# Kernel optimization log

Measured on AMD Instinct MI355X. Metric: run time of the kernel, lower is better.

## Reference

```python
import jax, jax.numpy as jnp
from jax import lax
import numpy as np

DN = ('NDHWC', 'DHWIO', 'NDHWC')

def conv3d(x, w, b, stride=1):
    return lax.conv_general_dilated(x, w, (stride,) * 3, 'SAME', dimension_numbers=DN) + b

def convT3d(x, w, b, stride=2):
    return lax.conv_transpose(x, w, (stride,) * 3, 'SAME', dimension_numbers=DN) + b

def prelu(x, a):
    return jnp.where(x > 0, x, a * x)

def bn(x, g, be, m, v):
    # keras BatchNormalization, inference mode, epsilon=1e-3
    return (x - m) * g * lax.rsqrt(v + 1e-3) + be

def res_unit(x, c1w, c1b, c2w, c2b, g, be, m, v, a):
    # VQVAEResidualUnit: relu(x + PReLU(BN(conv2(swish(conv1(x))))))
    h = jax.nn.swish(conv3d(x, c1w, c1b))
    h = prelu(bn(conv3d(h, c2w, c2b), g, be, m, v), a)
    return jax.nn.relu(x + h)

def _forward(x, ec0_w, ec0_b, er0_c1w, er0_c1b, er0_c2w, er0_c2b, er0_g, er0_be, er0_m, er0_v, er0_a, ec1_w, ec1_b, er1_c1w, er1_c1b, er1_c2w, er1_c2b, er1_g, er1_be, er1_m, er1_v, er1_a, eo_w, eo_b, eo_a, codebook, dc0_w, dc0_b, dc0_a, dr0_c1w, dr0_c1b, dr0_c2w, dr0_c2b, dr0_g, dr0_be, dr0_m, dr0_v, dr0_a, du0_w, du0_b, dr1_c1w, dr1_c1b, dr1_c2w, dr1_c2b, dr1_g, dr1_be, dr1_m, dr1_v, dr1_a, du1_w, du1_b):
    # ----- Encoder -----
    h = jax.nn.relu(conv3d(x, ec0_w, ec0_b, stride=2))   # [B,64,64,64,64]
    h = res_unit(h, er0_c1w, er0_c1b, er0_c2w, er0_c2b, er0_g, er0_be, er0_m, er0_v, er0_a)
    h = jax.nn.relu(conv3d(h, ec1_w, ec1_b, stride=2))   # [B,32,32,32,128]
    h = res_unit(h, er1_c1w, er1_c1b, er1_c2w, er1_c2b, er1_g, er1_be, er1_m, er1_v, er1_a)
    z = prelu(conv3d(h, eo_w, eo_b), eo_a)               # [B,32,32,32,64] latent
    # ----- NSVQ (inference: hard codebook lookup) -----
    D = z.shape[-1]
    flat = z.reshape(-1, D)                              # [N, 64], N = B*32^3
    dist = (flat * flat).sum(1, keepdims=True) + (codebook * codebook).sum(1) - 2.0 * (flat @ codebook.T)  # [N, K]
    idx = jnp.argmin(dist, axis=1)
    zq = codebook[idx].reshape(z.shape)
    K = codebook.shape[0]
    p = jnp.zeros((K,), jnp.float32).at[idx].add(1.0) / flat.shape[0]
    perplexity = jnp.exp(-jnp.sum(p * jnp.log(p + 1e-12)))
    # ----- Decoder -----
    h = prelu(conv3d(zq, dc0_w, dc0_b), dc0_a)           # [B,32,32,32,128]
    h = res_unit(h, dr0_c1w, dr0_c1b, dr0_c2w, dr0_c2b, dr0_g, dr0_be, dr0_m, dr0_v, dr0_a)
    h = jax.nn.relu(convT3d(h, du0_w, du0_b))            # [B,64,64,64,64]
    h = res_unit(h, dr1_c1w, dr1_c1b, dr1_c2w, dr1_c2b, dr1_g, dr1_be, dr1_m, dr1_v, dr1_a)
    recon = convT3d(h, du1_w, du1_b)                     # [B,128,128,128,1]
    return recon, perplexity

def setup_inputs() -> dict:
    key = jax.random.key(0)
    ks = iter(jax.random.split(key, 40))
    nrm = lambda *s: jax.random.normal(next(ks), s, jnp.float32) * 0.05
    def ru(pfx, c):
        return {pfx + '_c1w': nrm(3, 3, 3, c, c), pfx + '_c1b': jnp.zeros((c,), jnp.float32),
                pfx + '_c2w': nrm(3, 3, 3, c, c), pfx + '_c2b': jnp.zeros((c,), jnp.float32),
                pfx + '_g': jnp.ones((c,), jnp.float32), pfx + '_be': jnp.zeros((c,), jnp.float32),
                pfx + '_m': jnp.zeros((c,), jnp.float32), pfx + '_v': jnp.ones((c,), jnp.float32),
                pfx + '_a': jnp.full((c,), 0.25, jnp.float32)}
    C0, C1, D, K = 64, 128, 64, 512
    inp = {'x': jax.random.normal(next(ks), (2, 128, 128, 128, 1), jnp.float32)}
    inp.update(ec0_w=nrm(4, 4, 4, 1, C0), ec0_b=jnp.zeros((C0,), jnp.float32))
    inp.update(ru('er0', C0))
    inp.update(ec1_w=nrm(4, 4, 4, C0, C1), ec1_b=jnp.zeros((C1,), jnp.float32))
    inp.update(ru('er1', C1))
    inp.update(eo_w=nrm(3, 3, 3, C1, D), eo_b=jnp.zeros((D,), jnp.float32), eo_a=jnp.full((D,), 0.25, jnp.float32))
    inp.update(codebook=jax.random.uniform(next(ks), (K, D), jnp.float32, -1.0, 1.0) * np.sqrt(6.0 / D).astype(np.float32))
    inp.update(dc0_w=nrm(3, 3, 3, D, C1), dc0_b=jnp.zeros((C1,), jnp.float32), dc0_a=jnp.full((C1,), 0.25, jnp.float32))
    inp.update(ru('dr0', C1))
    inp.update(du0_w=nrm(4, 4, 4, C1, C0), du0_b=jnp.zeros((C0,), jnp.float32))
    inp.update(ru('dr1', C0))
    inp.update(du1_w=nrm(4, 4, 4, C0, 1), du1_b=jnp.zeros((1,), jnp.float32))
    return inp

def reference(x, ec0_w, ec0_b, er0_c1w, er0_c1b, er0_c2w, er0_c2b, er0_g, er0_be, er0_m, er0_v, er0_a, ec1_w, ec1_b, er1_c1w, er1_c1b, er1_c2w, er1_c2b, er1_g, er1_be, er1_m, er1_v, er1_a, eo_w, eo_b, eo_a, codebook, dc0_w, dc0_b, dc0_a, dr0_c1w, dr0_c1b, dr0_c2w, dr0_c2b, dr0_g, dr0_be, dr0_m, dr0_v, dr0_a, du0_w, du0_b, dr1_c1w, dr1_c1b, dr1_c2w, dr1_c2b, dr1_g, dr1_be, dr1_m, dr1_v, dr1_a, du1_w, du1_b):
    return _forward(x, ec0_w, ec0_b, er0_c1w, er0_c1b, er0_c2w, er0_c2b, er0_g, er0_be, er0_m, er0_v, er0_a, ec1_w, ec1_b, er1_c1w, er1_c1b, er1_c2w, er1_c2b, er1_g, er1_be, er1_m, er1_v, er1_a, eo_w, eo_b, eo_a, codebook, dc0_w, dc0_b, dc0_a, dr0_c1w, dr0_c1b, dr0_c2w, dr0_c2b, dr0_g, dr0_be, dr0_m, dr0_v, dr0_a, du0_w, du0_b, dr1_c1w, dr1_c1b, dr1_c2w, dr1_c2b, dr1_g, dr1_be, dr1_m, dr1_v, dr1_a, du1_w, du1_b)
```

## Files before the change

kernel.cpp:

```cpp
#include <hip/hip_runtime.h>
#include <cstdint>


typedef unsigned short bf16_t;
typedef __attribute__((ext_vector_type(8)))  short s8b;
typedef __attribute__((ext_vector_type(16))) float f32x16;

__device__ __forceinline__ float b2f(bf16_t u) { return __uint_as_float((unsigned)u << 16); }
__device__ __forceinline__ bf16_t f2b(float f) {
    unsigned x = __float_as_uint(f);
    return (bf16_t)((x + 0x7FFFu + ((x >> 16) & 1u)) >> 16);
}

__device__ __forceinline__ void split3s(float v, unsigned short& h,
                                        unsigned short& m, unsigned short& l)
{
    const unsigned uv = __float_as_uint(v);
    const float fh = __uint_as_float(uv & 0xFFFF0000u);
    const float r1 = v - fh;
    const unsigned u1 = __float_as_uint(r1);
    const float fm = __uint_as_float(u1 & 0xFFFF0000u);
    const float r2 = r1 - fm;
    h = (unsigned short)(uv >> 16);
    m = (unsigned short)(u1 >> 16);
// ... 8 lines not shown

__global__ __launch_bounds__(256)
void wprep3(const float* __restrict__ w, bf16_t* __restrict__ h,
            bf16_t* __restrict__ m, bf16_t* __restrict__ l,
            int ci, int co, int n)
{
    const int i = blockIdx.x * 256 + threadIdx.x;
    if (i >= n) return;
    const int co_ = i % co;
    const int ci_ = (i / co) % ci;
    const int tap = i / (co * ci);
    const int dst = wdst(tap, ci_, co_, ci, co);
    unsigned short hh, mm, ll2;
    split3s(w[i], hh, mm, ll2);
    h[dst] = hh; m[dst] = mm; l[dst] = ll2;
}

__global__ __launch_bounds__(256)
void wprep_split(const float* __restrict__ w, bf16_t* __restrict__ hi,
                 bf16_t* __restrict__ lo, int ci, int co, int n)
{
    const int i = blockIdx.x * 256 + threadIdx.x;
    if (i >= n) return;
    const int co_ = i % co;
    const int ci_ = (i / co) % ci;
    const int tap = i / (co * ci);
    const float v = w[i];
    const int dst = wdst(tap, ci_, co_, ci, co);
    const bf16_t h = f2b(v);
    hi[dst] = h;
    lo[dst] = f2b(v - b2f(h));
}

template<int CIN, int COUT, int SD, int NWC, int EPI>
__global__ __launch_bounds__((SD / 32) * NWC * 64)
void conv3e(const float* __restrict__ xf,
            const bf16_t* __restrict__ wh, const bf16_t* __restrict__ wm,
            const bf16_t* __restrict__ wl,
            const float* __restrict__ bias,
            const float* __restrict__ g, const float* __restrict__ be,
            const float* __restrict__ mn, const float* __restrict__ vr,
            const float* __restrict__ al,
            const float* skf, float* __restrict__ of)
{
    constexpr int NT = (SD / 32) * NWC * 64;
    constexpr int LP = (SD * CIN) / (4 * NT);
    constexpr int KS = CIN / 16;
    constexpr int RB = (SD + 2) * CIN;
    __shared__ bf16_t lh[2][RB], lm[2][RB], ll[2][RB];

    const int tid  = threadIdx.x;
    const int lane = tid & 63;
    const int wid  = tid >> 6;
    const int wn   = wid % NWC, wm2 = wid / NWC;
    const int half = lane >> 5, ln = lane & 31;
    const int w    = wm2 * 32 + ln;
    const int nwg  = gridDim.x;
    const int bid  = (blockIdx.x & 7) * (nwg >> 3) + (blockIdx.x >> 3);
    const int h    = bid % SD;
    const int d    = (bid / SD) % SD;
    const int b    = bid / (SD * SD);
    const int cout = wn * 32 + ln;

    int pz[9], py[9], pt[9], np = 0;
    for (int kd = 0; kd < 3; ++kd) {
        const int iz = d + kd - 1;
        if ((unsigned)iz >= (unsigned)SD) continue;
        for (int kh = 0; kh < 3; ++kh) {
            const int iy = h + kh - 1;
            if ((unsigned)iy >= (unsigned)SD) continue;
            pz[np] = iz; py[np] = iy; pt[np] = (kd * 3 + kh) * 3; ++np;
        }
    }

    f32x16 accA, accB;
#pragma unroll
    for (int i = 0; i < 16; ++i) { accA[i] = 0.f; accB[i] = 0.f; }

    for (int i = tid; i < CIN; i += NT) {
        const int bf2 = i / (CIN / 2);
        const int rem = i % (CIN / 2);
        const int pv = (rem < CIN / 4) ? 0 : (SD + 1);
        const int ch = (rem % (CIN / 4)) * 4;
        const int bo = ((pv * CIN + ch) * 2) ^ ((pv & 7) << 4);
        const ushort4 z4 = make_ushort4(0, 0, 0, 0);
        *reinterpret_cast<ushort4*>((char*)&lh[bf2][0] + bo) = z4;
        *reinterpret_cast<ushort4*>((char*)&lm[bf2][0] + bo) = z4;
        *reinterpret_cast<ushort4*>((char*)&ll[bf2][0] + bo) = z4;
    }

    float4 rg[LP];
    auto loadrow = [&](int iz, int iy) {
        const float* src = xf + ((size_t)((b * SD + iz) * SD + iy)) * SD * CIN;
#pragma unroll
        for (int j = 0; j < LP; ++j)
            rg[j] = *reinterpret_cast<const float4*>(src + (size_t)(tid + j * NT) * 4);
    };
    auto writerow = [&](int bf2) {
#pragma unroll
        for (int j = 0; j < LP; ++j) {
            const int idx = (tid + j * NT) * 4;
            const int pv = idx / CIN + 1, ch = idx % CIN;
            ushort4 h4, m4, l4;
            split3s(rg[j].x, h4.x, m4.x, l4.x);
            split3s(rg[j].y, h4.y, m4.y, l4.y);
            split3s(rg[j].z, h4.z, m4.z, l4.z);
            split3s(rg[j].w, h4.w, m4.w, l4.w);
            const int bo = ((pv * CIN + ch) * 2) ^ ((pv & 7) << 4);
            *reinterpret_cast<ushort4*>((char*)&lh[bf2][0] + bo) = h4;
            *reinterpret_cast<ushort4*>((char*)&lm[bf2][0] + bo) = m4;
            *reinterpret_cast<ushort4*>((char*)&ll[bf2][0] + bo) = l4;
        }
    };

    loadrow(pz[0], py[0]);
    writerow(0);
    if (np > 1) loadrow(pz[1], py[1]);
    __syncthreads();
#pragma unroll 1
    for (int i = 0; i < np; ++i) {
        const int cur = i & 1;
        if (i + 1 < np) writerow((i + 1) & 1);
        if (i + 2 < np) loadrow(pz[i + 2], py[i + 2]);
#pragma unroll
        for (int kw = 0; kw < 3; ++kw) {
            const int tap = pt[i] + kw;
            const int pv = w + kw;
#pragma unroll
            for (int ks = 0; ks < KS; ++ks) {
                const int bo = ((pv * CIN + half * 8 + ks * 16) * 2) ^ ((pv & 7) << 4);
                const s8b ah  = *reinterpret_cast<const s8b*>((const char*)&lh[cur][0] + bo);
                const s8b am  = *reinterpret_cast<const s8b*>((const char*)&lm[cur][0] + bo);
                const s8b al3 = *reinterpret_cast<const s8b*>((const char*)&ll[cur][0] + bo);
                const size_t wb = ((size_t)((tap * KS + ks) * 2 + half) * COUT + cout) * 8;
                const s8b bh = *reinterpret_cast<const s8b*>(wh + wb);
                const s8b bm = *reinterpret_cast<const s8b*>(wm + wb);
                const s8b bl = *reinterpret_cast<const s8b*>(wl + wb);
                accA = __builtin_amdgcn_mfma_f32_32x32x16_bf16(ah, bh, accA, 0, 0, 0);
                accB = __builtin_amdgcn_mfma_f32_32x32x16_bf16(ah, bm, accB, 0, 0, 0);
                accA = __builtin_amdgcn_mfma_f32_32x32x16_bf16(am, bh, accA, 0, 0, 0);
                accB = __builtin_amdgcn_mfma_f32_32x32x16_bf16(am, bm, accB, 0, 0, 0);
                accA = __builtin_amdgcn_mfma_f32_32x32x16_bf16(al3, bh, accA, 0, 0, 0);
                accB = __builtin_amdgcn_mfma_f32_32x32x16_bf16(ah, bl, accB, 0, 0, 0);
            }
        }
        __syncthreads();
    }

    const size_t outrow = ((size_t)((b * SD + d) * SD + h)) * SD;
    const float bv = bias[cout];
    float sc = 0.f, mm = 0.f, bb2 = 0.f, aa = 0.f;
    if constexpr (EPI == 3) {
        sc = g[cout] * (1.0f / sqrtf(vr[cout] + 1e-3f));
        mm = mn[cout]; bb2 = be[cout]; aa = al[cout];
    }
    if constexpr (EPI == 2) aa = al[cout];
#pragma unroll
    for (int r = 0; r < 16; ++r) {
        const int rl = (r & 3) + 8 * (r >> 2) + 4 * half;
        const size_t oe = (outrow + wm2 * 32 + rl) * COUT + cout;
        float y = accA[r] + accB[r] + bv;
        if constexpr (EPI == 0) y = fmaxf(y, 0.f);
        else if constexpr (EPI == 1) y = y / (1.f + expf(-y));
        else if constexpr (EPI == 2) y = y > 0.f ? y : aa * y;
        else {
            float t2 = (y - mm) * sc + bb2;
            t2 = t2 > 0.f ? t2 : aa * t2;
            y = fmaxf(skf[oe] + t2, 0.f);
        }
        of[oe] = y;
    }
}

__global__ __launch_bounds__(256)
void convs2e(const float* __restrict__ xf,
             const bf16_t* __restrict__ wh, const bf16_t* __restrict__ wm,
             const bf16_t* __restrict__ wl,
             const float* __restrict__ bias, float* __restrict__ of)
{
    constexpr int NT = 256, LP = (64 * 64) / (4 * NT);
    __shared__ bf16_t lh[2][66 * 64], lm[2][66 * 64], ll[2][66 * 64];

    const int tid  = threadIdx.x;
    const int lane = tid & 63;
    const int wn   = tid >> 6;
    const int half = lane >> 5, ln = lane & 31;
    const int nwg  = gridDim.x;
    const int bid  = (blockIdx.x & 7) * (nwg >> 3) + (blockIdx.x >> 3);
    const int h    = bid % 32;
    const int d    = (bid / 32) % 32;
    const int b    = bid / 1024;
    const int cout = wn * 32 + ln;

    int pz[16], py[16], pt[16], np = 0;
    for (int kd = 0; kd < 4; ++kd) {
        const int iz = 2 * d + kd - 1;
        if ((unsigned)iz >= 64u) continue;
        for (int kh = 0; kh < 4; ++kh) {
            const int iy = 2 * h + kh - 1;
            if ((unsigned)iy >= 64u) continue;
            pz[np] = iz; py[np] = iy; pt[np] = (kd * 4 + kh) * 4; ++np;
        }
    }

    f32x16 accA, accB;
#pragma unroll
    for (int i = 0; i < 16; ++i) { accA[i] = 0.f; accB[i] = 0.f; }

    for (int i = tid; i < 64; i += NT) {
        const int bf2 = i / 32;
        const int rem = i % 32;
        const int pv = (rem < 16) ? 0 : 65;
        const int ch = (rem % 16) * 4;
        const int bo = ((pv * 64 + ch) * 2) ^ ((pv & 7) << 4);
        const ushort4 z4 = make_ushort4(0, 0, 0, 0);
        *reinterpret_cast<ushort4*>((char*)&lh[bf2][0] + bo) = z4;
        *reinterpret_cast<ushort4*>((char*)&lm[bf2][0] + bo) = z4;
        *reinterpret_cast<ushort4*>((char*)&ll[bf2][0] + bo) = z4;
    }

    float4 rg[LP];
    auto loadrow = [&](int iz, int iy) {
        const float* src = xf + ((size_t)((b * 64 + iz) * 64 + iy)) * 64 * 64;
#pragma unroll
        for (int j = 0; j < LP; ++j)
            rg[j] = *reinterpret_cast<const float4*>(src + (size_t)(tid + j * NT) * 4);
    };
    auto writerow = [&](int bf2) {
#pragma unroll
        for (int j = 0; j < LP; ++j) {
            const int idx = (tid + j * NT) * 4;
            const int pv = idx / 64 + 1, ch = idx % 64;
            ushort4 h4, m4, l4;
            split3s(rg[j].x, h4.x, m4.x, l4.x);
            split3s(rg[j].y, h4.y, m4.y, l4.y);
            split3s(rg[j].z, h4.z, m4.z, l4.z);
            split3s(rg[j].w, h4.w, m4.w, l4.w);
            const int bo = ((pv * 64 + ch) * 2) ^ ((pv & 7) << 4);
            *reinterpret_cast<ushort4*>((char*)&lh[bf2][0] + bo) = h4;
            *reinterpret_cast<ushort4*>((char*)&lm[bf2][0] + bo) = m4;
            *reinterpret_cast<ushort4*>((char*)&ll[bf2][0] + bo) = l4;
        }
    };

    loadrow(pz[0], py[0]);
    writerow(0);
    if (np > 1) loadrow(pz[1], py[1]);
    __syncthreads();
#pragma unroll 1
    for (int i = 0; i < np; ++i) {
        const int cur = i & 1;
        if (i + 1 < np) writerow((i + 1) & 1);
        if (i + 2 < np) loadrow(pz[i + 2], py[i + 2]);
#pragma unroll
        for (int kw = 0; kw < 4; ++kw) {
            const int tap = pt[i] + kw;
            const int pv = 2 * ln + kw;
#pragma unroll
            for (int ks = 0; ks < 4; ++ks) {
                const int bo = ((pv * 64 + half * 8 + ks * 16) * 2) ^ ((pv & 7) << 4);
                const s8b ah  = *reinterpret_cast<const s8b*>((const char*)&lh[cur][0] + bo);
                const s8b am  = *reinterpret_cast<const s8b*>((const char*)&lm[cur][0] + bo);
                const s8b al3 = *reinterpret_cast<const s8b*>((const char*)&ll[cur][0] + bo);
                const size_t wb = ((size_t)((tap * 4 + ks) * 2 + half) * 128 + cout) * 8;
                const s8b bh = *reinterpret_cast<const s8b*>(wh + wb);
                const s8b bm = *reinterpret_cast<const s8b*>(wm + wb);
                const s8b bl = *reinterpret_cast<const s8b*>(wl + wb);
                accA = __builtin_amdgcn_mfma_f32_32x32x16_bf16(ah, bh, accA, 0, 0, 0);
                accB = __builtin_amdgcn_mfma_f32_32x32x16_bf16(ah, bm, accB, 0, 0, 0);
                accA = __builtin_amdgcn_mfma_f32_32x32x16_bf16(am, bh, accA, 0, 0, 0);
                accB = __builtin_amdgcn_mfma_f32_32x32x16_bf16(am, bm, accB, 0, 0, 0);
                accA = __builtin_amdgcn_mfma_f32_32x32x16_bf16(al3, bh, accA, 0, 0, 0);
                accB = __builtin_amdgcn_mfma_f32_32x32x16_bf16(ah, bl, accB, 0, 0, 0);
            }
        }
        __syncthreads();
    }

    const size_t outrow = ((size_t)((b * 32 + d) * 32 + h)) * 32;
    const float bv = bias[cout];
#pragma unroll
    for (int r = 0; r < 16; ++r) {
        const int rl = (r & 3) + 8 * (r >> 2) + 4 * half;
        const size_t oe = (outrow + rl) * 128 + cout;
        of[oe] = fmaxf(accA[r] + accB[r] + bv, 0.f);
    }
}

template<int CIN, int COUT, int SD, int NWC, int EPI>
__global__ __launch_bounds__((SD / 32) * NWC * 64)
void conv3d(const bf16_t* __restrict__ xh, const bf16_t* __restrict__ xl,
            const bf16_t* __restrict__ wh, const bf16_t* __restrict__ wl,
            const float* __restrict__ bias,
            const float* __restrict__ g, const float* __restrict__ be,
            const float* __restrict__ mn, const float* __restrict__ vr,
            const float* __restrict__ al,
            const bf16_t* skh, const bf16_t* skl,
            bf16_t* oh, bf16_t* ol)
{
    constexpr int NT = (SD / 32) * NWC * 64;
    constexpr int LP = (SD * CIN) / (4 * NT);
    constexpr int KS = CIN / 16;
    constexpr int RB = (SD + 2) * CIN;
    __shared__ bf16_t lh[2][RB], ll[2][RB];

    const int tid  = threadIdx.x;
    const int lane = tid & 63;
    const int wid  = tid >> 6;
    const int wn   = wid % NWC, wm2 = wid / NWC;
    const int half = lane >> 5, ln = lane & 31;
    const int w    = wm2 * 32 + ln;
    const int nwg  = gridDim.x;
    const int bid  = (blockIdx.x & 7) * (nwg >> 3) + (blockIdx.x >> 3);
    const int h    = bid % SD;
    const int d    = (bid / SD) % SD;
    const int b    = bid / (SD * SD);
    const int cout = wn * 32 + ln;

    int pz[9], py[9], pt[9], np = 0;
    for (int kd = 0; kd < 3; ++kd) {
        const int iz = d + kd - 1;
        if ((unsigned)iz >= (unsigned)SD) continue;
        for (int kh = 0; kh < 3; ++kh) {
            const int iy = h + kh - 1;
            if ((unsigned)iy >= (unsigned)SD) continue;
            pz[np] = iz; py[np] = iy; pt[np] = (kd * 3 + kh) * 3; ++np;
        }
    }

    f32x16 accA, accB;
#pragma unroll
    for (int i = 0; i < 16; ++i) { accA[i] = 0.f; accB[i] = 0.f; }

    for (int i = tid; i < CIN; i += NT) {
        const int bf2 = i / (CIN / 2);
        const int rem = i % (CIN / 2);
        const int pv = (rem < CIN / 4) ? 0 : (SD + 1);
        const int ch = (rem % (CIN / 4)) * 4;
        const int bo = ((pv * CIN + ch) * 2) ^ ((pv & 7) << 4);
        const ushort4 z4 = make_ushort4(0, 0, 0, 0);
        *reinterpret_cast<ushort4*>((char*)&lh[bf2][0] + bo) = z4;
        *reinterpret_cast<ushort4*>((char*)&ll[bf2][0] + bo) = z4;
    }

    ushort4 rh[LP], rl2a[LP];
    auto loadrow = [&](int iz, int iy) {
        const size_t rb = ((size_t)((b * SD + iz) * SD + iy)) * SD * CIN;
#pragma unroll
        for (int j = 0; j < LP; ++j) {
            const int idx = (tid + j * NT) * 4;
            rh[j]   = *reinterpret_cast<const ushort4*>(xh + rb + idx);
            rl2a[j] = *reinterpret_cast<const ushort4*>(xl + rb + idx);
        }
    };
    auto writerow = [&](int bf2) {
#pragma unroll
        for (int j = 0; j < LP; ++j) {
            const int idx = (tid + j * NT) * 4;
            const int pv = idx / CIN + 1, ch = idx % CIN;
            const int bo = ((pv * CIN + ch) * 2) ^ ((pv & 7) << 4);
            *reinterpret_cast<ushort4*>((char*)&lh[bf2][0] + bo) = rh[j];
            *reinterpret_cast<ushort4*>((char*)&ll[bf2][0] + bo) = rl2a[j];
        }
    };

    loadrow(pz[0], py[0]);
    writerow(0);
    if (np > 1) loadrow(pz[1], py[1]);
    __syncthreads();
#pragma unroll 1
    for (int i = 0; i < np; ++i) {
        const int cur = i & 1;
        if (i + 1 < np) writerow((i + 1) & 1);
        if (i + 2 < np) loadrow(pz[i + 2], py[i + 2]);
#pragma unroll
        for (int kw = 0; kw < 3; ++kw) {
            const int tap = pt[i] + kw;
            const int pv = w + kw;
#pragma unroll
            for (int ks = 0; ks < KS; ++ks) {
                const int bo = ((pv * CIN + half * 8 + ks * 16) * 2) ^ ((pv & 7) << 4);
                const s8b ah  = *reinterpret_cast<const s8b*>((const char*)&lh[cur][0] + bo);
                const s8b al2 = *reinterpret_cast<const s8b*>((const char*)&ll[cur][0] + bo);
                const size_t wb = ((size_t)((tap * KS + ks) * 2 + half) * COUT + cout) * 8;
                const s8b bh = *reinterpret_cast<const s8b*>(wh + wb);
                const s8b bl = *reinterpret_cast<const s8b*>(wl + wb);
                accA = __builtin_amdgcn_mfma_f32_32x32x16_bf16(ah, bh, accA, 0, 0, 0);
                accB = __builtin_amdgcn_mfma_f32_32x32x16_bf16(al2, bh, accB, 0, 0, 0);
                accB = __builtin_amdgcn_mfma_f32_32x32x16_bf16(ah, bl, accB, 0, 0, 0);
            }
        }
        __syncthreads();
    }

    const size_t outrow = ((size_t)((b * SD + d) * SD + h)) * SD;
    const float bv = bias[cout];
    float sc = 0.f, mm = 0.f, bb2 = 0.f, aa = 0.f;
    if constexpr (EPI == 3) {
        sc = g[cout] * (1.0f / sqrtf(vr[cout] + 1e-3f));
        mm = mn[cout]; bb2 = be[cout]; aa = al[cout];
    }
    if constexpr (EPI == 2) aa = al[cout];
#pragma unroll
    for (int r = 0; r < 16; ++r) {
        const int rl3 = (r & 3) + 8 * (r >> 2) + 4 * half;
        const size_t oe = (outrow + wm2 * 32 + rl3) * COUT + cout;
        float y = accA[r] + accB[r] + bv;
        if constexpr (EPI == 0) y = fmaxf(y, 0.f);
        else if constexpr (EPI == 1) y = y / (1.f + expf(-y));
        else if constexpr (EPI == 2) y = y > 0.f ? y : aa * y;
        else {
            float t2 = (y - mm) * sc + bb2;
            t2 = t2 > 0.f ? t2 : aa * t2;
            float sv = b2f(skh[oe]) + b2f(skl[oe]);
            y = fmaxf(sv + t2, 0.f);
        }
        const bf16_t hh = f2b(y);
        oh[oe] = hh;
        ol[oe] = f2b(y - b2f(hh));
    }
}

__global__ __launch_bounds__(256)
void convTm(const bf16_t* __restrict__ xh, const bf16_t* __restrict__ xl,
            const bf16_t* __restrict__ wh, const bf16_t* __restrict__ wl,
            const float* __restrict__ bias,
            bf16_t* __restrict__ oh, bf16_t* __restrict__ ol)
{
    constexpr int NT = 256, LP = (32 * 128) / (4 * NT);
    __shared__ bf16_t lh[2][34 * 128], ll[2][34 * 128];

    const int tid  = threadIdx.x;
    const int lane = tid & 63;
    const int wid  = tid >> 6;
    const int wn   = wid & 1, p = wid >> 1;
    const int half = lane >> 5, ln = lane & 31;
    const int nwg  = gridDim.x;
    const int bid  = (blockIdx.x & 7) * (nwg >> 3) + (blockIdx.x >> 3);
    const int ohh  = bid % 64;
    const int od   = (bid / 64) % 64;
    const int b    = bid / 4096;
    const int pd = od & 1, dz = od >> 1;
    const int ph = ohh & 1, hy = ohh >> 1;
    const int cout = wn * 32 + ln;

    int pz[4], py[4], pt[4], np = 0;
    for (int jd = 0; jd < 2; ++jd) {
        const int kd = pd + 2 * jd;
        const int iz = dz + pd - 1 + jd;
        if ((unsigned)iz >= 32u) continue;
        for (int jh = 0; jh < 2; ++jh) {
            const int kh = ph + 2 * jh;
            const int iy = hy + ph - 1 + jh;
            if ((unsigned)iy >= 32u) continue;
            pz[np] = iz; py[np] = iy; pt[np] = (kd * 4 + kh) * 4; ++np;
        }
    }

    f32x16 accA, accB;
#pragma unroll
    for (int i = 0; i < 16; ++i) { accA[i] = 0.0f; accB[i] = 0.0f; }

    for (int i = tid; i < 128; i += NT) {
        const int bf2 = i / 64;
        const int rem = i % 64;
        const int pv = (rem < 32) ? 0 : 33;
        const int ch = (rem % 32) * 4;
        const int bo = ((pv * 128 + ch) * 2) ^ ((pv & 7) << 4);
        const ushort4 z4 = make_ushort4(0, 0, 0, 0);
        *reinterpret_cast<ushort4*>((char*)&lh[bf2][0] + bo) = z4;
        *reinterpret_cast<ushort4*>((char*)&ll[bf2][0] + bo) = z4;
    }

    ushort4 rh[LP], rl2a[LP];
    auto loadrow = [&](int iz, int iy) {
        const size_t rb = ((size_t)((b * 32 + iz) * 32 + iy)) * 32 * 128;
#pragma unroll
        for (int j = 0; j < LP; ++j) {
            const int idx = (tid + j * NT) * 4;
            rh[j]   = *reinterpret_cast<const ushort4*>(xh + rb + idx);
            rl2a[j] = *reinterpret_cast<const ushort4*>(xl + rb + idx);
        }
    };
    auto writerow = [&](int bf2) {
#pragma unroll
        for (int j = 0; j < LP; ++j) {
            const int idx = (tid + j * NT) * 4;
            const int pv = idx / 128 + 1, ch = idx % 128;
            const int bo = ((pv * 128 + ch) * 2) ^ ((pv & 7) << 4);
            *reinterpret_cast<ushort4*>((char*)&lh[bf2][0] + bo) = rh[j];
            *reinterpret_cast<ushort4*>((char*)&ll[bf2][0] + bo) = rl2a[j];
        }
    };

    loadrow(pz[0], py[0]);
    writerow(0);
    if (np > 1) loadrow(pz[1], py[1]);
    __syncthreads();
#pragma unroll 1
    for (int i = 0; i < np; ++i) {
        const int cur = i & 1;
        if (i + 1 < np) writerow((i + 1) & 1);
        if (i + 2 < np) loadrow(pz[i + 2], py[i + 2]);
#pragma unroll
        for (int jw = 0; jw < 2; ++jw) {
            const int kw = p + 2 * jw;
            const int tap = pt[i] + kw;
            const int pv = ln + p + jw;
#pragma unroll
            for (int ks = 0; ks < 8; ++ks) {
                const int bo = ((pv * 128 + half * 8 + ks * 16) * 2) ^ ((pv & 7) << 4);
                const s8b a  = *reinterpret_cast<const s8b*>((const char*)&lh[cur][0] + bo);
                const s8b a2 = *reinterpret_cast<const s8b*>((const char*)&ll[cur][0] + bo);
                const size_t wb = ((size_t)((tap * 8 + ks) * 2 + half) * 64 + cout) * 8;
                const s8b bb = *reinterpret_cast<const s8b*>(wh + wb);
                const s8b b2 = *reinterpret_cast<const s8b*>(wl + wb);
                accA = __builtin_amdgcn_mfma_f32_32x32x16_bf16(a, bb, accA, 0, 0, 0);
                accB = __builtin_amdgcn_mfma_f32_32x32x16_bf16(a2, bb, accB, 0, 0, 0);
                accB = __builtin_amdgcn_mfma_f32_32x32x16_bf16(a, b2, accB, 0, 0, 0);
            }
        }
        __syncthreads();
    }

    const float bv = bias[cout];
#pragma unroll
    for (int r = 0; r < 16; ++r) {
        const int rl3 = (r & 3) + 8 * (r >> 2) + 4 * half;
        const int ow = 2 * rl3 + p;
        const size_t oe = (((size_t)((b * 64 + od) * 64 + ohh)) * 64 + ow) * 64 + cout;
        const float y = fmaxf(accA[r] + accB[r] + bv, 0.f);
        const bf16_t hh = f2b(y);
        oh[oe] = hh;
        ol[oe] = f2b(y - b2f(hh));
    }
}

__global__ __launch_bounds__(128)
void conv_ec0m(const float* __restrict__ x,
               const bf16_t* __restrict__ wh, const bf16_t* __restrict__ wm,
               const bf16_t* __restrict__ wl,
               const float* __restrict__ bias, float* __restrict__ of)
{
    __shared__ bf16_t lh[16 * 132], lm[16 * 132], ll[16 * 132];

    const int tid  = threadIdx.x;
    const int lane = tid & 63;
    const int wm2  = tid >> 6;
    const int half = lane >> 5, ln = lane & 31;
    const int w    = wm2 * 32 + ln;
    const int nwg  = gridDim.x;
    const int bid  = (blockIdx.x & 7) * (nwg >> 3) + (blockIdx.x >> 3);
    const int h    = bid % 64;
    const int d    = (bid / 64) % 64;
    const int b    = bid / 4096;

    for (int i = tid; i < 16 * 132; i += 128) {
        const int row = i / 132, col = i % 132;
        const int kd = row >> 2, kh = row & 3;
        const int iz = 2 * d + kd - 1, iy = 2 * h + kh - 1;
        const int ix = col - 1;
        float v = 0.f;
        if ((unsigned)iz < 128u && (unsigned)iy < 128u &&
            (unsigned)ix < 128u && col < 130)
            v = x[(size_t)((b * 128 + iz) * 128 + iy) * 128 + ix];
        unsigned short hh, mm2, ll2;
        split3s(v, hh, mm2, ll2);
// ... 317 lines not shown
    bf16_t* e1c2l = (bf16_t*)(WB + 8896512);
    bf16_t* eoh   = (bf16_t*)(WB + 9781248);
    bf16_t* eom   = (bf16_t*)(WB + 10223616);
    bf16_t* eol   = (bf16_t*)(WB + 10665984);
    bf16_t* wec0h = (bf16_t*)(WB + 11108352);
    bf16_t* wec0m = (bf16_t*)(WB + 11116544);
    bf16_t* wec0l = (bf16_t*)(WB + 11124736);
    bf16_t* dc0h  = (bf16_t*)(WB + 0);
    bf16_t* dc0l  = (bf16_t*)(WB + 442368);
    bf16_t* d0c1h = (bf16_t*)(WB + 884736);
    bf16_t* d0c1l = (bf16_t*)(WB + 1769472);
    bf16_t* d0c2h = (bf16_t*)(WB + 2654208);
    bf16_t* d0c2l = (bf16_t*)(WB + 3538944);
    bf16_t* du0h  = (bf16_t*)(WB + 4423680);
    bf16_t* du0l  = (bf16_t*)(WB + 5472256);
    bf16_t* d1c1h = (bf16_t*)(WB + 6520832);
    bf16_t* d1c1l = (bf16_t*)(WB + 6742016);
    bf16_t* d1c2h = (bf16_t*)(WB + 6963200);
    bf16_t* d1c2l = (bf16_t*)(WB + 7184384);

    const float* fn = nullptr;
    const bf16_t* bn_ = nullptr;

    wprep3<<<16, 256, 0, stream>>>(ec0_w, wec0h, wec0m, wec0l, 64, 64, 4096);
    wprep3<<<432, 256, 0, stream>>>(er0_c1w, e0c1h, e0c1m, e0c1l, 64, 64, 110592);
    wprep3<<<432, 256, 0, stream>>>(er0_c2w, e0c2h, e0c2m, e0c2l, 64, 64, 110592);
    wprep3<<<2048, 256, 0, stream>>>(ec1_w, ec1h, ec1m, ec1l, 64, 128, 524288);
    wprep3<<<1728, 256, 0, stream>>>(er1_c1w, e1c1h, e1c1m, e1c1l, 128, 128, 442368);
    wprep3<<<1728, 256, 0, stream>>>(er1_c2w, e1c2h, e1c2m, e1c2l, 128, 128, 442368);
    wprep3<<<864, 256, 0, stream>>>(eo_w, eoh, eom, eol, 128, 64, 221184);

    conv_ec0m<<<8192, 128, 0, stream>>>(x, wec0h, wec0m, wec0l, ec0_b, Af);

    conv3e<64, 64, 64, 2, 1><<<8192, 256, 0, stream>>>(
        Af, e0c1h, e0c1m, e0c1l, er0_c1b, fn, fn, fn, fn, fn, fn, Hf);
    conv3e<64, 64, 64, 2, 3><<<8192, 256, 0, stream>>>(
        Hf, e0c2h, e0c2m, e0c2l, er0_c2b, er0_g, er0_be, er0_m, er0_v, er0_a, Af, Af);

    convs2e<<<2048, 256, 0, stream>>>(Af, ec1h, ec1m, ec1l, ec1_b, E1f);

    conv3e<128, 128, 32, 4, 1><<<2048, 256, 0, stream>>>(
        E1f, e1c1h, e1c1m, e1c1l, er1_c1b, fn, fn, fn, fn, fn, fn, R1f);
    conv3e<128, 128, 32, 4, 3><<<2048, 256, 0, stream>>>(
        R1f, e1c2h, e1c2m, e1c2l, er1_c2b, er1_g, er1_be, er1_m, er1_v, er1_a, E1f, E1f);

    conv3e<128, 64, 32, 2, 2><<<2048, 128, 0, stream>>>(
        E1f, eoh, eom, eol, eo_b, fn, fn, fn, fn, eo_a, fn, Zf);

    vq_cnorm<<<8, 64, 0, stream>>>(cb, CN);
    zero512<<<1, 512, 0, stream>>>(HS);
    vq_assign<<<256, 256, 0, stream>>>(Zf, cb, CN, IDX, HS, 65536);
    perplexity_k<<<1, 512, 0, stream>>>(HS, out + 4194304, 1.0f / 65536.0f);
    vq_gather_split<<<4096, 256, 0, stream>>>(cb, IDX, ZQh, ZQl);

    wprep_split<<<864, 256, 0, stream>>>(dc0_w, dc0h, dc0l, 64, 128, 221184);
    wprep_split<<<1728, 256, 0, stream>>>(dr0_c1w, d0c1h, d0c1l, 128, 128, 442368);
    wprep_split<<<1728, 256, 0, stream>>>(dr0_c2w, d0c2h, d0c2l, 128, 128, 442368);
    wprep_split<<<2048, 256, 0, stream>>>(du0_w, du0h, du0l, 128, 64, 524288);
    wprep_split<<<432, 256, 0, stream>>>(dr1_c1w, d1c1h, d1c1l, 64, 64, 110592);
    wprep_split<<<432, 256, 0, stream>>>(dr1_c2w, d1c2h, d1c2l, 64, 64, 110592);

    conv3d<64, 128, 32, 4, 2><<<2048, 256, 0, stream>>>(
        ZQh, ZQl, dc0h, dc0l, dc0_b, fn, fn, fn, fn, dc0_a, bn_, bn_, D0h, D0l);
    conv3d<128, 128, 32, 4, 1><<<2048, 256, 0, stream>>>(
        D0h, D0l, d0c1h, d0c1l, dr0_c1b, fn, fn, fn, fn, fn, bn_, bn_, Gh, Gl);
    conv3d<128, 128, 32, 4, 3><<<2048, 256, 0, stream>>>(
        Gh, Gl, d0c2h, d0c2l, dr0_c2b, dr0_g, dr0_be, dr0_m, dr0_v, dr0_a,
        D0h, D0l, D0h, D0l);

    convTm<<<8192, 256, 0, stream>>>(D0h, D0l, du0h, du0l, du0_b, U0h, U0l);

    conv3d<64, 64, 64, 2, 1><<<8192, 256, 0, stream>>>(
        U0h, U0l, d1c1h, d1c1l, dr1_c1b, fn, fn, fn, fn, fn, bn_, bn_, G1h, G1l);
    conv3d<64, 64, 64, 2, 3><<<8192, 256, 0, stream>>>(
        G1h, G1l, d1c2h, d1c2l, dr1_c2b, dr1_g, dr1_be, dr1_m, dr1_v, dr1_a,
        U0h, U0l, U0h, U0l);

    convT_du1w<<<65536, 256, 0, stream>>>(U0h, U0l, du1_w, du1_b, out);
}
```

Baseline: 5.127 ms.

## Compute two 32-channel output tiles per wave to reuse LDS A-fragments

Each wave in the conv kernels now accumulates two 32-wide output-channel tiles (NC2) instead of one, and block sizes are halved to keep the same total channel coverage. Each activation fragment read from LDS then feeds twice as many MFMAs, which cuts LDS read traffic and halves the number of threads staging each input row. In exchange each wave holds twice as many accumulator registers, which may lower occupancy. The smaller blocks also mean fewer threads share the global-to-LDS row loads.

```diff
diff --git a/kernel.cpp b/kernel.cpp
--- a/kernel.cpp
+++ b/kernel.cpp
@@ -64,8 +64,8 @@
     lo[dst] = f2b(v - b2f(h));
 }
 
-template<int CIN, int COUT, int SD, int NWC, int EPI>
-__global__ __launch_bounds__((SD / 32) * NWC * 64)
+template<int CIN, int COUT, int SD, int NW, int EPI>
+__global__ __launch_bounds__((SD / 32) * NW * 64)
 void conv3e(const float* __restrict__ xf,
             const bf16_t* __restrict__ wh, const bf16_t* __restrict__ wm,
             const bf16_t* __restrict__ wl,
@@ -75,16 +75,17 @@
             const float* __restrict__ al,
             const float* skf, float* __restrict__ of)
 {
-    constexpr int NT = (SD / 32) * NWC * 64;
-    constexpr int LP = (SD * CIN) / (4 * NT);
-    constexpr int KS = CIN / 16;
-    constexpr int RB = (SD + 2) * CIN;
+    constexpr int NT  = (SD / 32) * NW * 64;
+    constexpr int LP  = (SD * CIN) / (4 * NT);
+    constexpr int KS  = CIN / 16;
+    constexpr int NC2 = COUT / (32 * NW);
+    constexpr int RB  = (SD + 2) * CIN;
     __shared__ bf16_t lh[2][RB], lm[2][RB], ll[2][RB];
 
     const int tid  = threadIdx.x;
     const int lane = tid & 63;
     const int wid  = tid >> 6;
-    const int wn   = wid % NWC, wm2 = wid / NWC;
+    const int wn   = wid % NW, wm2 = wid / NW;
     const int half = lane >> 5, ln = lane & 31;
     const int w    = wm2 * 32 + ln;
     const int nwg  = gridDim.x;
@@ -92,7 +93,7 @@
     const int h    = bid % SD;
     const int d    = (bid / SD) % SD;
     const int b    = bid / (SD * SD);
-    const int cout = wn * 32 + ln;
+    const int cout0 = wn * (NC2 * 32) + ln;
 
     int pz[9], py[9], pt[9], np = 0;
     for (int kd = 0; kd < 3; ++kd) {
@@ -105,9 +106,11 @@
         }
     }
 
-    f32x16 accA, accB;
-#pragma unroll
-    for (int i = 0; i < 16; ++i) { accA[i] = 0.f; accB[i] = 0.f; }
+    f32x16 accA[NC2], accB[NC2];
+#pragma unroll
+    for (int c = 0; c < NC2; ++c)
+#pragma unroll
+        for (int i = 0; i < 16; ++i) { accA[c][i] = 0.f; accB[c][i] = 0.f; }
 
     for (int i = tid; i < CIN; i += NT) {
         const int bf2 = i / (CIN / 2);
@@ -164,53 +167,61 @@
                 const s8b ah  = *reinterpret_cast<const s8b*>((const char*)&lh[cur][0] + bo);
                 const s8b am  = *reinterpret_cast<const s8b*>((const char*)&lm[cur][0] + bo);
                 const s8b al3 = *reinterpret_cast<const s8b*>((const char*)&ll[cur][0] + bo);
-                const size_t wb = ((size_t)((tap * KS + ks) * 2 + half) * COUT + cout) * 8;
-                const s8b bh = *reinterpret_cast<const s8b*>(wh + wb);
-                const s8b bm = *reinterpret_cast<const s8b*>(wm + wb);
-                const s8b bl = *reinterpret_cast<const s8b*>(wl + wb);
-                accA = __builtin_amdgcn_mfma_f32_32x32x16_bf16(ah, bh, accA, 0, 0, 0);
-                accB = __builtin_amdgcn_mfma_f32_32x32x16_bf16(ah, bm, accB, 0, 0, 0);
-                accA = __builtin_amdgcn_mfma_f32_32x32x16_bf16(am, bh, accA, 0, 0, 0);
-                accB = __builtin_amdgcn_mfma_f32_32x32x16_bf16(am, bm, accB, 0, 0, 0);
-                accA = __builtin_amdgcn_mfma_f32_32x32x16_bf16(al3, bh, accA, 0, 0, 0);
-                accB = __builtin_amdgcn_mfma_f32_32x32x16_bf16(ah, bl, accB, 0, 0, 0);
+                const size_t wb0 = ((size_t)((tap * KS + ks) * 2 + half) * COUT + cout0) * 8;
+#pragma unroll
+                for (int c = 0; c < NC2; ++c) {
+                    const size_t wb = wb0 + (size_t)c * 256;
+                    const s8b bh = *reinterpret_cast<const s8b*>(wh + wb);
+                    const s8b bm = *reinterpret_cast<const s8b*>(wm + wb);
+                    const s8b bl = *reinterpret_cast<const s8b*>(wl + wb);
+                    accA[c] = __builtin_amdgcn_mfma_f32_32x32x16_bf16(ah, bh, accA[c], 0, 0, 0);
+                    accB[c] = __builtin_amdgcn_mfma_f32_32x32x16_bf16(ah, bm, accB[c], 0, 0, 0);
+                    accA[c] = __builtin_amdgcn_mfma_f32_32x32x16_bf16(am, bh, accA[c], 0, 0, 0);
+                    accB[c] = __builtin_amdgcn_mfma_f32_32x32x16_bf16(am, bm, accB[c], 0, 0, 0);
+                    accA[c] = __builtin_amdgcn_mfma_f32_32x32x16_bf16(al3, bh, accA[c], 0, 0, 0);
+                    accB[c] = __builtin_amdgcn_mfma_f32_32x32x16_bf16(ah, bl, accB[c], 0, 0, 0);
+                }
             }
         }
         __syncthreads();
     }
 
     const size_t outrow = ((size_t)((b * SD + d) * SD + h)) * SD;
-    const float bv = bias[cout];
-    float sc = 0.f, mm = 0.f, bb2 = 0.f, aa = 0.f;
-    if constexpr (EPI == 3) {
-        sc = g[cout] * (1.0f / sqrtf(vr[cout] + 1e-3f));
-        mm = mn[cout]; bb2 = be[cout]; aa = al[cout];
-    }
-    if constexpr (EPI == 2) aa = al[cout];
-#pragma unroll
-    for (int r = 0; r < 16; ++r) {
-        const int rl = (r & 3) + 8 * (r >> 2) + 4 * half;
-        const size_t oe = (outrow + wm2 * 32 + rl) * COUT + cout;
-        float y = accA[r] + accB[r] + bv;
-        if constexpr (EPI == 0) y = fmaxf(y, 0.f);
-        else if constexpr (EPI == 1) y = y / (1.f + expf(-y));
-        else if constexpr (EPI == 2) y = y > 0.f ? y : aa * y;
-        else {
-            float t2 = (y - mm) * sc + bb2;
-            t2 = t2 > 0.f ? t2 : aa * t2;
-            y = fmaxf(skf[oe] + t2, 0.f);
-        }
-        of[oe] = y;
-    }
-}
-
-__global__ __launch_bounds__(256)
+#pragma unroll
+    for (int c = 0; c < NC2; ++c) {
+        const int cout = cout0 + c * 32;
+        const float bv = bias[cout];
+        float sc = 0.f, mm = 0.f, bb2 = 0.f, aa = 0.f;
+        if constexpr (EPI == 3) {
+            sc = g[cout] * (1.0f / sqrtf(vr[cout] + 1e-3f));
+            mm = mn[cout]; bb2 = be[cout]; aa = al[cout];
+        }
+        if constexpr (EPI == 2) aa = al[cout];
+#pragma unroll
+        for (int r = 0; r < 16; ++r) {
+            const int rl = (r & 3) + 8 * (r >> 2) + 4 * half;
+            const size_t oe = (outrow + wm2 * 32 + rl) * COUT + cout;
+            float y = accA[c][r] + accB[c][r] + bv;
+            if constexpr (EPI == 0) y = fmaxf(y, 0.f);
+            else if constexpr (EPI == 1) y = y / (1.f + expf(-y));
+            else if constexpr (EPI == 2) y = y > 0.f ? y : aa * y;
+            else {
+                float t2 = (y - mm) * sc + bb2;
+                t2 = t2 > 0.f ? t2 : aa * t2;
+                y = fmaxf(skf[oe] + t2, 0.f);
+            }
+            of[oe] = y;
+        }
+    }
+}
+
+__global__ __launch_bounds__(128)
 void convs2e(const float* __restrict__ xf,
              const bf16_t* __restrict__ wh, const bf16_t* __restrict__ wm,
              const bf16_t* __restrict__ wl,
              const float* __restrict__ bias, float* __restrict__ of)
 {
-    constexpr int NT = 256, LP = (64 * 64) / (4 * NT);
+    constexpr int NT = 128, LP = (64 * 64) / (4 * NT);
     __shared__ bf16_t lh[2][66 * 64], lm[2][66 * 64], ll[2][66 * 64];
 
     const int tid  = threadIdx.x;
@@ -222,7 +233,7 @@
     const int h    = bid % 32;
     const int d    = (bid / 32) % 32;
     const int b    = bid / 1024;
-    const int cout = wn * 32 + ln;
+    const int cout0 = wn * 64 + ln;
 
     int pz[16], py[16], pt[16], np = 0;
     for (int kd = 0; kd < 4; ++kd) {
@@ -235,9 +246,12 @@
         }
     }
 
-    f32x16 accA, accB;
-#pragma unroll
-    for (int i = 0; i < 16; ++i) { accA[i] = 0.f; accB[i] = 0.f; }
+    f32x16 accA[2], accB[2];
+#pragma unroll
+    for (int i = 0; i < 16; ++i) {
+        accA[0][i] = 0.f; accA[1][i] = 0.f;
+        accB[0][i] = 0.f; accB[1][i] = 0.f;
+    }
 
     for (int i = tid; i < 64; i += NT) {
         const int bf2 = i / 32;
@@ -294,33 +308,41 @@
                 const s8b ah  = *reinterpret_cast<const s8b*>((const char*)&lh[cur][0] + bo);
                 const s8b am  = *reinterpret_cast<const s8b*>((const char*)&lm[cur][0] + bo);
                 const s8b al3 = *reinterpret_cast<const s8b*>((const char*)&ll[cur][0] + bo);
-                const size_t wb = ((size_t)((tap * 4 + ks) * 2 + half) * 128 + cout) * 8;
-                const s8b bh = *reinterpret_cast<const s8b*>(wh + wb);
-                const s8b bm = *reinterpret_cast<const s8b*>(wm + wb);
-                const s8b bl = *reinterpret_cast<const s8b*>(wl + wb);
-                accA = __builtin_amdgcn_mfma_f32_32x32x16_bf16(ah, bh, accA, 0, 0, 0);
-                accB = __builtin_amdgcn_mfma_f32_32x32x16_bf16(ah, bm, accB, 0, 0, 0);
-                accA = __builtin_amdgcn_mfma_f32_32x32x16_bf16(am, bh, accA, 0, 0, 0);
-                accB = __builtin_amdgcn_mfma_f32_32x32x16_bf16(am, bm, accB, 0, 0, 0);
-                accA = __builtin_amdgcn_mfma_f32_32x32x16_bf16(al3, bh, accA, 0, 0, 0);
-                accB = __builtin_amdgcn_mfma_f32_32x32x16_bf16(ah, bl, accB, 0, 0, 0);
+                const size_t wb0 = ((size_t)((tap * 4 + ks) * 2 + half) * 128 + cout0) * 8;
+#pragma unroll
+                for (int c = 0; c < 2; ++c) {
+                    const size_t wb = wb0 + (size_t)c * 256;
+                    const s8b bh = *reinterpret_cast<const s8b*>(wh + wb);
+                    const s8b bm = *reinterpret_cast<const s8b*>(wm + wb);
+                    const s8b bl = *reinterpret_cast<const s8b*>(wl + wb);
+                    accA[c] = __builtin_amdgcn_mfma_f32_32x32x16_bf16(ah, bh, accA[c], 0, 0, 0);
+                    accB[c] = __builtin_amdgcn_mfma_f32_32x32x16_bf16(ah, bm, accB[c], 0, 0, 0);
+                    accA[c] = __builtin_amdgcn_mfma_f32_32x32x16_bf16(am, bh, accA[c], 0, 0, 0);
+                    accB[c] = __builtin_amdgcn_mfma_f32_32x32x16_bf16(am, bm, accB[c], 0, 0, 0);
+                    accA[c] = __builtin_amdgcn_mfma_f32_32x32x16_bf16(al3, bh, accA[c], 0, 0, 0);
+                    accB[c] = __builtin_amdgcn_mfma_f32_32x32x16_bf16(ah, bl, accB[c], 0, 0, 0);
+                }
             }
         }
         __syncthreads();
     }
 
     const size_t outrow = ((size_t)((b * 32 + d) * 32 + h)) * 32;
-    const float bv = bias[cout];
-#pragma unroll
-    for (int r = 0; r < 16; ++r) {
-        const int rl = (r & 3) + 8 * (r >> 2) + 4 * half;
-        const size_t oe = (outrow + rl) * 128 + cout;
-        of[oe] = fmaxf(accA[r] + accB[r] + bv, 0.f);
-    }
-}
-
-template<int CIN, int COUT, int SD, int NWC, int EPI>
-__global__ __launch_bounds__((SD / 32) * NWC * 64)
+#pragma unroll
+    for (int c = 0; c < 2; ++c) {
+        const int cout = cout0 + c * 32;
+        const float bv = bias[cout];
+#pragma unroll
+        for (int r = 0; r < 16; ++r) {
+            const int rl = (r & 3) + 8 * (r >> 2) + 4 * half;
+            const size_t oe = (outrow + rl) * 128 + cout;
+            of[oe] = fmaxf(accA[c][r] + accB[c][r] + bv, 0.f);
+        }
+    }
+}
+
+template<int CIN, int COUT, int SD, int NW, int EPI>
+__global__ __launch_bounds__((SD / 32) * NW * 64)
 void conv3d(const bf16_t* __restrict__ xh, const bf16_t* __restrict__ xl,
             const bf16_t* __restrict__ wh, const bf16_t* __restrict__ wl,
             const float* __restrict__ bias,
@@ -330,16 +352,17 @@
             const bf16_t* skh, const bf16_t* skl,
             bf16_t* oh, bf16_t* ol)
 {
-    constexpr int NT = (SD / 32) * NWC * 64;
-    constexpr int LP = (SD * CIN) / (4 * NT);
-    constexpr int KS = CIN / 16;
-    constexpr int RB = (SD + 2) * CIN;
+    constexpr int NT  = (SD / 32) * NW * 64;
+    constexpr int LP  = (SD * CIN) / (4 * NT);
+    constexpr int KS  = CIN / 16;
+    constexpr int NC2 = COUT / (32 * NW);
+    constexpr int RB  = (SD + 2) * CIN;
     __shared__ bf16_t lh[2][RB], ll[2][RB];
 
     const int tid  = threadIdx.x;
     const int lane = tid & 63;
     const int wid  = tid >> 6;
-    const int wn   = wid % NWC, wm2 = wid / NWC;
+    const int wn   = wid % NW, wm2 = wid / NW;
     const int half = lane >> 5, ln = lane & 31;
     const int w    = wm2 * 32 + ln;
     const int nwg  = gridDim.x;
@@ -347,7 +370,7 @@
     const int h    = bid % SD;
     const int d    = (bid / SD) % SD;
     const int b    = bid / (SD * SD);
-    const int cout = wn * 32 + ln;
+    const int cout0 = wn * (NC2 * 32) + ln;
 
     int pz[9], py[9], pt[9], np = 0;
     for (int kd = 0; kd < 3; ++kd) {
@@ -360,9 +383,11 @@
         }
     }
 
-    f32x16 accA, accB;
-#pragma unroll
-    for (int i = 0; i < 16; ++i) { accA[i] = 0.f; accB[i] = 0.f; }
+    f32x16 accA[NC2], accB[NC2];
+#pragma unroll
+    for (int c = 0; c < NC2; ++c)
+#pragma unroll
+        for (int i = 0; i < 16; ++i) { accA[c][i] = 0.f; accB[c][i] = 0.f; }
 
     for (int i = tid; i < CIN; i += NT) {
         const int bf2 = i / (CIN / 2);
@@ -414,58 +439,65 @@
                 const int bo = ((pv * CIN + half * 8 + ks * 16) * 2) ^ ((pv & 7) << 4);
                 const s8b ah  = *reinterpret_cast<const s8b*>((const char*)&lh[cur][0] + bo);
                 const s8b al2 = *reinterpret_cast<const s8b*>((const char*)&ll[cur][0] + bo);
-                const size_t wb = ((size_t)((tap * KS + ks) * 2 + half) * COUT + cout) * 8;
-                const s8b bh = *reinterpret_cast<const s8b*>(wh + wb);
-                const s8b bl = *reinterpret_cast<const s8b*>(wl + wb);
-                accA = __builtin_amdgcn_mfma_f32_32x32x16_bf16(ah, bh, accA, 0, 0, 0);
-                accB = __builtin_amdgcn_mfma_f32_32x32x16_bf16(al2, bh, accB, 0, 0, 0);
-                accB = __builtin_amdgcn_mfma_f32_32x32x16_bf16(ah, bl, accB, 0, 0, 0);
+                const size_t wb0 = ((size_t)((tap * KS + ks) * 2 + half) * COUT + cout0) * 8;
+#pragma unroll
+                for (int c = 0; c < NC2; ++c) {
+                    const size_t wb = wb0 + (size_t)c * 256;
+                    const s8b bh = *reinterpret_cast<const s8b*>(wh + wb);
+                    const s8b bl = *reinterpret_cast<const s8b*>(wl + wb);
+                    accA[c] = __builtin_amdgcn_mfma_f32_32x32x16_bf16(ah, bh, accA[c], 0, 0, 0);
+                    accB[c] = __builtin_amdgcn_mfma_f32_32x32x16_bf16(al2, bh, accB[c], 0, 0, 0);
+                    accB[c] = __builtin_amdgcn_mfma_f32_32x32x16_bf16(ah, bl, accB[c], 0, 0, 0);
+                }
             }
         }
         __syncthreads();
     }
 
     const size_t outrow = ((size_t)((b * SD + d) * SD + h)) * SD;
-    const float bv = bias[cout];
-    float sc = 0.f, mm = 0.f, bb2 = 0.f, aa = 0.f;
-    if constexpr (EPI == 3) {
-        sc = g[cout] * (1.0f / sqrtf(vr[cout] + 1e-3f));
-        mm = mn[cout]; bb2 = be[cout]; aa = al[cout];
-    }
-    if constexpr (EPI == 2) aa = al[cout];
-#pragma unroll
-    for (int r = 0; r < 16; ++r) {
-        const int rl3 = (r & 3) + 8 * (r >> 2) + 4 * half;
-        const size_t oe = (outrow + wm2 * 32 + rl3) * COUT + cout;
-        float y = accA[r] + accB[r] + bv;
-        if constexpr (EPI == 0) y = fmaxf(y, 0.f);
-        else if constexpr (EPI == 1) y = y / (1.f + expf(-y));
-        else if constexpr (EPI == 2) y = y > 0.f ? y : aa * y;
-        else {
-            float t2 = (y - mm) * sc + bb2;
-            t2 = t2 > 0.f ? t2 : aa * t2;
-            float sv = b2f(skh[oe]) + b2f(skl[oe]);
-            y = fmaxf(sv + t2, 0.f);
-        }
-        const bf16_t hh = f2b(y);
-        oh[oe] = hh;
-        ol[oe] = f2b(y - b2f(hh));
-    }
-}
-
-__global__ __launch_bounds__(256)
+#pragma unroll
+    for (int c = 0; c < NC2; ++c) {
+        const int cout = cout0 + c * 32;
+        const float bv = bias[cout];
+        float sc = 0.f, mm = 0.f, bb2 = 0.f, aa = 0.f;
+        if constexpr (EPI == 3) {
+            sc = g[cout] * (1.0f / sqrtf(vr[cout] + 1e-3f));
+            mm = mn[cout]; bb2 = be[cout]; aa = al[cout];
+        }
+        if constexpr (EPI == 2) aa = al[cout];
+#pragma unroll
+        for (int r = 0; r < 16; ++r) {
+            const int rl3 = (r & 3) + 8 * (r >> 2) + 4 * half;
+            const size_t oe = (outrow + wm2 * 32 + rl3) * COUT + cout;
+            float y = accA[c][r] + accB[c][r] + bv;
+            if constexpr (EPI == 0) y = fmaxf(y, 0.f);
+            else if constexpr (EPI == 1) y = y / (1.f + expf(-y));
+            else if constexpr (EPI == 2) y = y > 0.f ? y : aa * y;
+            else {
+                float t2 = (y - mm) * sc + bb2;
+                t2 = t2 > 0.f ? t2 : aa * t2;
+                float sv = b2f(skh[oe]) + b2f(skl[oe]);
+                y = fmaxf(sv + t2, 0.f);
+            }
+            const bf16_t hh = f2b(y);
+            oh[oe] = hh;
+            ol[oe] = f2b(y - b2f(hh));
+        }
+    }
+}
+
+__global__ __launch_bounds__(128)
 void convTm(const bf16_t* __restrict__ xh, const bf16_t* __restrict__ xl,
             const bf16_t* __restrict__ wh, const bf16_t* __restrict__ wl,
             const float* __restrict__ bias,
             bf16_t* __restrict__ oh, bf16_t* __restrict__ ol)
 {
-    constexpr int NT = 256, LP = (32 * 128) / (4 * NT);
+    constexpr int NT = 128, LP = (32 * 128) / (4 * NT);
     __shared__ bf16_t lh[2][34 * 128], ll[2][34 * 128];
 
     const int tid  = threadIdx.x;
     const int lane = tid & 63;
-    const int wid  = tid >> 6;
-    const int wn   = wid & 1, p = wid >> 1;
+    const int p    = tid >> 6;
     const int half = lane >> 5, ln = lane & 31;
     const int nwg  = gridDim.x;
     const int bid  = (blockIdx.x & 7) * (nwg >> 3) + (blockIdx.x >> 3);
@@ -474,7 +506,6 @@
     const int b    = bid / 4096;
     const int pd = od & 1, dz = od >> 1;
     const int ph = ohh & 1, hy = ohh >> 1;
-    const int cout = wn * 32 + ln;
 
     int pz[4], py[4], pt[4], np = 0;
     for (int jd = 0; jd < 2; ++jd) {
@@ -489,9 +520,12 @@
         }
     }
 
-    f32x16 accA, accB;
-#pragma unroll
-    for (int i = 0; i < 16; ++i) { accA[i] = 0.0f; accB[i] = 0.0f; }
+    f32x16 accA[2], accB[2];
+#pragma unroll
+    for (int i = 0; i < 16; ++i) {
+        accA[0][i] = 0.f; accA[1][i] = 0.f;
+        accB[0][i] = 0.f; accB[1][i] = 0.f;
+    }
 
     for (int i = tid; i < 128; i += NT) {
         const int bf2 = i / 64;
@@ -544,27 +578,35 @@
                 const int bo = ((pv * 128 + half * 8 + ks * 16) * 2) ^ ((pv & 7) << 4);
                 const s8b a  = *reinterpret_cast<const s8b*>((const char*)&lh[cur][0] + bo);
                 const s8b a2 = *reinterpret_cast<const s8b*>((const char*)&ll[cur][0] + bo);
-                const size_t wb = ((size_t)((tap * 8 + ks) * 2 + half) * 64 + cout) * 8;
-                const s8b bb = *reinterpret_cast<const s8b*>(wh + wb);
-                const s8b b2 = *reinterpret_cast<const s8b*>(wl + wb);
-                accA = __builtin_amdgcn_mfma_f32_32x32x16_bf16(a, bb, accA, 0, 0, 0);
-                accB = __builtin_amdgcn_mfma_f32_32x32x16_bf16(a2, bb, accB, 0, 0, 0);
-                accB = __builtin_amdgcn_mfma_f32_32x32x16_bf16(a, b2, accB, 0, 0, 0);
+                const size_t wb0 = ((size_t)((tap * 8 + ks) * 2 + half) * 64 + ln) * 8;
+#pragma unroll
+                for (int c = 0; c < 2; ++c) {
+                    const size_t wb = wb0 + (size_t)c * 256;
+                    const s8b bb = *reinterpret_cast<const s8b*>(wh + wb);
+                    const s8b b2 = *reinterpret_cast<const s8b*>(wl + wb);
+                    accA[c] = __builtin_amdgcn_mfma_f32_32x32x16_bf16(a, bb, accA[c], 0, 0, 0);
+                    accB[c] = __builtin_amdgcn_mfma_f32_32x32x16_bf16(a2, bb, accB[c], 0, 0, 0);
+                    accB[c] = __builtin_amdgcn_mfma_f32_32x32x16_bf16(a, b2, accB[c], 0, 0, 0);
+                }
             }
         }
         __syncthreads();
     }
 
-    const float bv = bias[cout];
-#pragma unroll
-    for (int r = 0; r < 16; ++r) {
-        const int rl3 = (r & 3) + 8 * (r >> 2) + 4 * half;
-        const int ow = 2 * rl3 + p;
-        const size_t oe = (((size_t)((b * 64 + od) * 64 + ohh)) * 64 + ow) * 64 + cout;
-        const float y = fmaxf(accA[r] + accB[r] + bv, 0.f);
-        const bf16_t hh = f2b(y);
-        oh[oe] = hh;
-        ol[oe] = f2b(y - b2f(hh));
+#pragma unroll
+    for (int c = 0; c < 2; ++c) {
+        const int cout = c * 32 + ln;
+        const float bv = bias[cout];
+#pragma unroll
+        for (int r = 0; r < 16; ++r) {
+            const int rl3 = (r & 3) + 8 * (r >> 2) + 4 * half;
+            const int ow = 2 * rl3 + p;
+            const size_t oe = (((size_t)((b * 64 + od) * 64 + ohh)) * 64 + ow) * 64 + cout;
+            const float y = fmaxf(accA[c][r] + accB[c][r] + bv, 0.f);
+            const bf16_t hh = f2b(y);
+            oh[oe] = hh;
+            ol[oe] = f2b(y - b2f(hh));
+        }
     }
 }
 
@@ -948,16 +990,16 @@
 
     conv_ec0m<<<8192, 128, 0, stream>>>(x, wec0h, wec0m, wec0l, ec0_b, Af);
 
-    conv3e<64, 64, 64, 2, 1><<<8192, 256, 0, stream>>>(
+    conv3e<64, 64, 64, 1, 1><<<8192, 128, 0, stream>>>(
         Af, e0c1h, e0c1m, e0c1l, er0_c1b, fn, fn, fn, fn, fn, fn, Hf);
-    conv3e<64, 64, 64, 2, 3><<<8192, 256, 0, stream>>>(
+    conv3e<64, 64, 64, 1, 3><<<8192, 128, 0, stream>>>(
         Hf, e0c2h, e0c2m, e0c2l, er0_c2b, er0_g, er0_be, er0_m, er0_v, er0_a, Af, Af);
 
-    convs2e<<<2048, 256, 0, stream>>>(Af, ec1h, ec1m, ec1l, ec1_b, E1f);
-
-    conv3e<128, 128, 32, 4, 1><<<2048, 256, 0, stream>>>(
+    convs2e<<<2048, 128, 0, stream>>>(Af, ec1h, ec1m, ec1l, ec1_b, E1f);
+
+    conv3e<128, 128, 32, 2, 1><<<2048, 128, 0, stream>>>(
         E1f, e1c1h, e1c1m, e1c1l, er1_c1b, fn, fn, fn, fn, fn, fn, R1f);
-    conv3e<128, 128, 32, 4, 3><<<2048, 256, 0, stream>>>(
+    conv3e<128, 128, 32, 2, 3><<<2048, 128, 0, stream>>>(
         R1f, e1c2h, e1c2m, e1c2l, er1_c2b, er1_g, er1_be, er1_m, er1_v, er1_a, E1f, E1f);
 
     conv3e<128, 64, 32, 2, 2><<<2048, 128, 0, stream>>>(
@@ -976,19 +1018,19 @@
     wprep_split<<<432, 256, 0, stream>>>(dr1_c1w, d1c1h, d1c1l, 64, 64, 110592);
     wprep_split<<<432, 256, 0, stream>>>(dr1_c2w, d1c2h, d1c2l, 64, 64, 110592);
 
-    conv3d<64, 128, 32, 4, 2><<<2048, 256, 0, stream>>>(
+    conv3d<64, 128, 32, 2, 2><<<2048, 128, 0, stream>>>(
         ZQh, ZQl, dc0h, dc0l, dc0_b, fn, fn, fn, fn, dc0_a, bn_, bn_, D0h, D0l);
-    conv3d<128, 128, 32, 4, 1><<<2048, 256, 0, stream>>>(
+    conv3d<128, 128, 32, 2, 1><<<2048, 128, 0, stream>>>(
         D0h, D0l, d0c1h, d0c1l, dr0_c1b, fn, fn, fn, fn, fn, bn_, bn_, Gh, Gl);
-    conv3d<128, 128, 32, 4, 3><<<2048, 256, 0, stream>>>(
+    conv3d<128, 128, 32, 2, 3><<<2048, 128, 0, stream>>>(
         Gh, Gl, d0c2h, d0c2l, dr0_c2b, dr0_g, dr0_be, dr0_m, dr0_v, dr0_a,
         D0h, D0l, D0h, D0l);
 
-    convTm<<<8192, 256, 0, stream>>>(D0h, D0l, du0h, du0l, du0_b, U0h, U0l);
-
-    conv3d<64, 64, 64, 2, 1><<<8192, 256, 0, stream>>>(
+    convTm<<<8192, 128, 0, stream>>>(D0h, D0l, du0h, du0l, du0_b, U0h, U0l);
+
+    conv3d<64, 64, 64, 1, 1><<<8192, 128, 0, stream>>>(
         U0h, U0l, d1c1h, d1c1l, dr1_c1b, fn, fn, fn, fn, fn, bn_, bn_, G1h, G1l);
-    conv3d<64, 64, 64, 2, 3><<<8192, 256, 0, stream>>>(
+    conv3d<64, 64, 64, 1, 3><<<8192, 128, 0, stream>>>(
         G1h, G1l, d1c2h, d1c2l, dr1_c2b, dr1_g, dr1_be, dr1_m, dr1_v, dr1_a,
         U0h, U0l, U0h, U0l);
 
```

New measurement: 5.549 ms. 8.2% more time.
